# Kernel tuning notes

Hardware: AMD Instinct MI355X
Metric: run time of the kernel (lower is better)

The kernel has to match this reference:

```python
import jax, jax.numpy as jnp
import numpy as np

DIM = 768
NUM_HEADS = 12
N_DIV = 8
T_SHIFT = 20
T_SPAN = 11
T_CUT = T_SHIFT + 1 - T_SPAN  # 10
C = DIM // NUM_HEADS          # 64 channels per head
FOLD = C // N_DIV             # 8
BATCH = 2
FRAMES = 32
K_WIN = 4
N_TOK = 196
B_TOT = BATCH * FRAMES * K_WIN  # 256


def _entmax15_last(x):
    """Exact entmax-1.5 (Peters & Martins) along the last axis."""
    x = (x - jnp.max(x, axis=-1, keepdims=True)) * 0.5
    xs = jnp.flip(jnp.sort(x, axis=-1), axis=-1)  # descending
    d = x.shape[-1]
    rho = jnp.arange(1, d + 1, dtype=x.dtype)
    mean = jnp.cumsum(xs, axis=-1) / rho
    meansq = jnp.cumsum(xs * xs, axis=-1) / rho
    ss = rho * (meansq - mean * mean)
    delta = (1.0 - ss) / rho
    pos = delta > 0
    sq = jnp.where(pos, jnp.sqrt(jnp.where(pos, delta, 1.0)), 0.0)
    tau = mean - sq
    support = jnp.sum(tau <= xs, axis=-1, keepdims=True)
    tau_star = jnp.take_along_axis(tau, support - 1, axis=-1)
    y = jnp.clip(x - tau_star, 0.0, None)
    return y * y


def entmax15(x, axis):
    return jnp.moveaxis(_entmax15_last(jnp.moveaxis(x, axis, -1)), -1, axis)


def _shift(feat, pool_w, pool_b, win_w, win_b, forward):
    # feat: [b, t, k, h, n, c]
    b, t, k, h, n, c = feat.shape
    f = N_DIV
    cp = c // f
    # 'b t k h n (c f) -> (k n h c) (b f) t'
    g = feat.reshape(b, t, k, h, n, cp, f)
    g = jnp.transpose(g, (2, 4, 3, 5, 0, 6, 1)).reshape(k * n * h * cp, b * f, t)
    pad = (T_SHIFT, 0) if forward else (0, T_SHIFT)
    g = jnp.pad(g, ((0, 0), (0, 0), pad))
    # 'b t k h n c -> b (k n t) (h c)'
    xk = jnp.transpose(feat, (0, 2, 4, 1, 3, 5)).reshape(b, k * n * t, h * c)
    attn = xk @ pool_w + pool_b                      # [b, knt, 1]
    pooled = jnp.sum(entmax15(attn, axis=1) * xk, axis=1)  # [b, dim]
    # 'b 1 (T f) -> (b f) 1 T'
    win = (pooled @ win_w + win_b).reshape(b, T_SPAN, f)
    win = jnp.transpose(win, (0, 2, 1)).reshape(b * f, 1, T_SPAN)
    win = _entmax15_last(win)
    # depthwise conv over the (b f) channel dim, batch dim = k*n*h*cp
    out = jax.lax.conv_general_dilated(
        g, win, (1,), 'VALID',
        dimension_numbers=('NCH', 'OIH', 'NCH'),
        feature_group_count=b * f)
    tp = t + T_CUT
    # '(k n h c) (b f) t -> b t k h n c f' then mean over f
    out = out.reshape(k, n, h, cp, b, f, tp)
    out = jnp.transpose(out, (4, 6, 0, 2, 1, 3, 5)).mean(axis=-1)  # [b, tp, k, h, n, cp]
    return out[:, :-T_CUT] if forward else out[:, T_CUT:]


def _pcs(x, batch_size, frame_len, fpw, fpb, bpw, bpb, fww, fwb, bww, bwb):
    B, h, n, c = x.shape
    k = B // (batch_size * frame_len)
    feat = x.reshape(batch_size, frame_len, k, h, n, c)
    fwd = _shift(feat, fpw, fpb, fww, fwb, True)
    bwd = _shift(feat, bpw, bpb, bww, bwb, False)
    out = jnp.concatenate([fwd, bwd, feat[..., 2 * FOLD:]], axis=-1)
    return out.reshape(B, h, n, c)


def setup_inputs() -> dict:
    key = jax.random.key(0)
    ks = jax.random.split(key, 6)
    s = 0.02
    return {
        'x': jax.random.normal(ks[0], (B_TOT, NUM_HEADS, N_TOK, C), dtype=jnp.float32),
        'batch_size': BATCH,
        'frame_len': FRAMES,
        'fwd_pool_w': jax.random.normal(ks[1], (DIM, 1), dtype=jnp.float32) * s,
        'fwd_pool_b': jnp.zeros((1,), dtype=jnp.float32),
        'bwd_pool_w': jax.random.normal(ks[2], (DIM, 1), dtype=jnp.float32) * s,
        'bwd_pool_b': jnp.zeros((1,), dtype=jnp.float32),
        'fwd_win_w': jax.random.normal(ks[3], (DIM, T_SPAN * N_DIV), dtype=jnp.float32) * s,
        'fwd_win_b': jnp.zeros((T_SPAN * N_DIV,), dtype=jnp.float32),
        'bwd_win_w': jax.random.normal(ks[4], (DIM, T_SPAN * N_DIV), dtype=jnp.float32) * s,
        'bwd_win_b': jnp.zeros((T_SPAN * N_DIV,), dtype=jnp.float32),
    }


def reference(x, batch_size, frame_len, fwd_pool_w, fwd_pool_b, bwd_pool_w, bwd_pool_b,
              fwd_win_w, fwd_win_b, bwd_win_w, bwd_win_b):
    return _pcs(x, batch_size, frame_len, fwd_pool_w, fwd_pool_b, bwd_pool_w, bwd_pool_b,
                fwd_win_w, fwd_win_b, bwd_win_w, bwd_win_b)
```

## Files before the change

kernel.cpp:

```cpp
#include <hip/hip_runtime.h>

#define NH 12
#define NTOK 196
#define TT 32
#define KW 4
#define NI 25088
#define TSTRIDE 602112

typedef float nfloat4 __attribute__((ext_vector_type(4)));

__global__ __launch_bounds__(256) void k_attn(
    const float4* __restrict__ x4, const float4* __restrict__ wf4,
    const float4* __restrict__ wb4, float* __restrict__ attn,
    float4* __restrict__ out4)
{
  int B = blockIdx.y;
  int wave = threadIdx.x >> 6, lane = threadIdx.x & 63;
  int n = blockIdx.x * 16 + wave * 4 + (lane >> 4);
  int c4 = lane & 15;
  bool nv = (n < NTOK);
  float accf = 0.f, accb = 0.f;
  #pragma unroll
  for (int h = 0; h < NH; h++) {
    float4 xv = make_float4(0.f, 0.f, 0.f, 0.f);
    int gi = ((B * NH + h) * NTOK + n) * 16 + c4;
    if (nv) xv = x4[gi];
    float4 wf = wf4[h * 16 + c4];
    float4 wb = wb4[h * 16 + c4];
    accf += xv.x * wf.x + xv.y * wf.y + xv.z * wf.z + xv.w * wf.w;
    accb += xv.x * wb.x + xv.y * wb.y + xv.z * wb.z + xv.w * wb.w;
    if (nv && c4 >= 4) {
      nfloat4 nv4 = { xv.x, xv.y, xv.z, xv.w };
      __builtin_nontemporal_store(nv4, (nfloat4*)&out4[gi]);
    }
  }
  #pragma unroll
  for (int m = 1; m < 16; m <<= 1) {
    accf += __shfl_xor(accf, m);
    accb += __shfl_xor(accb, m);
  }
  if (nv && (lane & 15) == 0) {
    int b = B >> 7, t = (B >> 2) & 31, k = B & 3;
    int i = (k * NTOK + n) * TT + t;
    attn[(0 * 2 + b) * NI + i] = accf;
    attn[(1 * 2 + b) * NI + i] = accb;
  }
}

__global__ __launch_bounds__(1024) void k_entmax_big(
    const float* __restrict__ attn, float* __restrict__ wgt,
    int* __restrict__ idxb, int* __restrict__ cnt)
{
  int p = blockIdx.x;
  const float* a = attn + p * NI;
  int tid = threadIdx.x;
  float v[25];
  float mx = -3.0e38f;
  #pragma unroll
  for (int r = 0; r < 25; r++) {
    int i = r * 1024 + tid;
    v[r] = (i < NI) ? a[i] : -3.0e38f;
    mx = fmaxf(mx, v[r]);
  }
  __shared__ float sred1[16];
  __shared__ float sred2[16];
  __shared__ float sbc;
  int wv = tid >> 6;
  #pragma unroll
  for (int m = 1; m < 64; m <<= 1) mx = fmaxf(mx, __shfl_xor(mx, m));
  if ((tid & 63) == 0) sred1[wv] = mx;
  __syncthreads();
  if (tid == 0) {
    float m2 = sred1[0];
    for (int i2 = 1; i2 < 16; i2++) m2 = fmaxf(m2, sred1[i2]);
    sbc = m2;
  }
  __syncthreads();
  float amax = sbc;
  #pragma unroll
  for (int r = 0; r < 25; r++) v[r] = 0.5f * (v[r] - amax);
  float tau = -1.0f;
  for (int it = 0; it < 8; it++) {
    float s2 = 0.f, s1 = 0.f;
    #pragma unroll
    for (int r = 0; r < 25; r++) {
      float d = fmaxf(v[r] - tau, 0.f);
      s2 += d * d;
      s1 += d;
    }
    #pragma unroll
    for (int m = 1; m < 64; m <<= 1) {
      s2 += __shfl_xor(s2, m);
      s1 += __shfl_xor(s1, m);
    }
    if ((tid & 63) == 0) { sred2[wv] = s2; sred1[wv] = s1; }
    __syncthreads();
    if (tid == 0) {
      float S2 = 0.f, S1 = 0.f;
      for (int i2 = 0; i2 < 16; i2++) { S2 += sred2[i2]; S1 += sred1[i2]; }
      sbc = tau + (S2 - 1.f) / fmaxf(2.f * S1, 1e-12f);
    }
    __syncthreads();
    tau = sbc;
    __syncthreads();
  }
  #pragma unroll
  for (int r = 0; r < 25; r++) {
    float d = v[r] - tau;
    if (d > 0.f) {
      int i = r * 1024 + tid;
      int slot = atomicAdd(&cnt[p], 1);
      idxb[p * NI + slot] = i;
      wgt[p * NI + slot] = d * d;
    }
  }
}

__global__ __launch_bounds__(256) void k_pool(
    const float* __restrict__ x, const int* __restrict__ idxb,
    const float* __restrict__ wgt, const int* __restrict__ cnt,
    float* __restrict__ pooled)
{
  int p = blockIdx.x >> 3, stripe = blockIdx.x & 7;
  int b = p & 1;
  int wv = threadIdx.x >> 6, lane = threadIdx.x & 63;
  int count = cnt[p];
  float acc[12];
  #pragma unroll
  for (int q = 0; q < 12; q++) acc[q] = 0.f;
  for (int e = stripe * 4 + wv; e < count; e += 32) {
    int i = idxb[p * NI + e];
    float pw = wgt[p * NI + e];
    int t = i & 31, r = i >> 5;
    int n = r % NTOK, k = r / NTOK;
    int B = (b * TT + t) * KW + k;
    const float* xb = x + B * 150528 + n * 64 + lane;
    #pragma unroll
    for (int q = 0; q < 12; q++) acc[q] += pw * xb[q * 12544];
  }
  #pragma unroll
  for (int q = 0; q < 12; q++)
    atomicAdd(&pooled[p * 768 + q * 64 + lane], acc[q]);
}

__global__ __launch_bounds__(384) void k_win(
    const float* __restrict__ pooled,
    const float* __restrict__ fww, const float* __restrict__ fwb,
    const float* __restrict__ bww, const float* __restrict__ bwb,
    float* __restrict__ winout)
{
  __shared__ float praw[4][88];
  int tid = threadIdx.x;
  if (tid < 352) {
    int p = tid / 88, col = tid % 88;
    const float* ww = (p >> 1) ? bww : fww;
    const float* wb = (p >> 1) ? bwb : fwb;
    float acc = wb[col];
    const float* pl = pooled + p * 768;
    #pragma unroll 8
    for (int r = 0; r < 768; r++) acc += pl[r] * ww[r * 88 + col];
    praw[p][col] = acc;
  }
  __syncthreads();
  if (tid < 32) {
    int p = tid >> 3, f = tid & 7;
    float v[11];
    float mx = -3.0e38f;
    #pragma unroll
    for (int j = 0; j < 11; j++) { v[j] = praw[p][j * 8 + f]; mx = fmaxf(mx, v[j]); }
    #pragma unroll
    for (int j = 0; j < 11; j++) v[j] = 0.5f * (v[j] - mx);
    float lo = -1.f, hi = 0.f;
    for (int it = 0; it < 30; it++) {
      float mid = 0.5f * (lo + hi);
      float s = 0.f;
      #pragma unroll
      for (int j = 0; j < 11; j++) { float d = fmaxf(v[j] - mid, 0.f); s += d * d; }
      if (s >= 1.f) lo = mid; else hi = mid;
    }
    float tau = 0.5f * (lo + hi);
    #pragma unroll
    for (int j = 0; j < 11; j++) {
      float d = fmaxf(v[j] - tau, 0.f);
      winout[p * 88 + f * 11 + j] = d * d * 0.125f;
    }
  }
}

__global__ __launch_bounds__(256) void k_shift(
    const float* __restrict__ x, const float* __restrict__ win,
    float* __restrict__ out)
{
  int bkh = blockIdx.y;
  int b = bkh / 48, rem = bkh % 48;
  int k = rem / 12, h = rem % 12;
  int wave = threadIdx.x >> 6, lane = threadIdx.x & 63;
  int n = blockIdx.x * 4 + wave;
  int f = lane & 7, cp = lane >> 3;
  float wjf[11], wjb[11];
  #pragma unroll
  for (int j = 0; j < 11; j++) {
    wjf[j] = win[(0 * 2 + b) * 88 + f * 11 + j];
    wjb[j] = win[(1 * 2 + b) * 88 + f * 11 + j];
  }
  int base = ((b * 128 + k) * NH + h) * 12544 + n * 64 + cp * 8 + f;
  float xr[32];
  #pragma unroll
  for (int tp = 0; tp < 32; tp++) xr[tp] = x[base + tp * TSTRIDE];

  int ob = ((b * 128 + k) * NH + h) * 12544 + n * 64 + cp;
  float acc[32];

  #pragma unroll
  for (int t = 0; t < 32; t++) acc[t] = 0.f;
  #pragma unroll
  for (int tp = 0; tp <= 21; tp++) {
    #pragma unroll
    for (int j = 0; j < 11; j++) {
      int to = tp + 20 - j;
      if (to >= 0 && to < 32) acc[to] += wjf[j] * xr[tp];
    }
  }
  #pragma unroll
  for (int t = 0; t < 32; t++) {
    float s = acc[t];
    s += __shfl_xor(s, 1);
    s += __shfl_xor(s, 2);
    s += __shfl_xor(s, 4);
    acc[t] = s;
  }
  if (f == 0) {
    #pragma unroll
    for (int t = 0; t < 32; t++)
      __builtin_nontemporal_store(acc[t], &out[ob + t * TSTRIDE]);
  }

  #pragma unroll
  for (int t = 0; t < 32; t++) acc[t] = 0.f;
  #pragma unroll
  for (int tp = 10; tp < 32; tp++) {
    #pragma unroll
    for (int j = 0; j < 11; j++) {
      int to = tp - 10 - j;
      if (to >= 0 && to < 32) acc[to] += wjb[j] * xr[tp];
    }
  }
  #pragma unroll
  for (int t = 0; t < 32; t++) {
    float s = acc[t];
    s += __shfl_xor(s, 1);
    s += __shfl_xor(s, 2);
    s += __shfl_xor(s, 4);
    acc[t] = s;
  }
  if (f == 0) {
    #pragma unroll
    for (int t = 0; t < 32; t++)
      __builtin_nontemporal_store(acc[t], &out[ob + 8 + t * TSTRIDE]);
  }
}

extern "C" void kernel_launch(void* const* d_in, const int* in_sizes, int n_in,
                              void* d_out, int out_size, void* d_ws, size_t ws_size,
                              hipStream_t stream)
{
  (void)in_sizes; (void)n_in; (void)out_size; (void)ws_size;
  const float* x   = (const float*)d_in[0];
  const float* fpw = (const float*)d_in[3];
  const float* bpw = (const float*)d_in[5];
  const float* fww = (const float*)d_in[7];
  const float* fwb = (const float*)d_in[8];
  const float* bww = (const float*)d_in[9];
  const float* bwb = (const float*)d_in[10];
  float* out = (float*)d_out;

  float* W      = (float*)d_ws;
  int*   cnt    = (int*)W;
  float* pooled = W + 4;
  float* attn   = W + 4 + 3072;
  float* wgt    = attn + 4 * NI;
  int*   idxb   = (int*)(wgt + 4 * NI);
  float* winb   = (float*)(idxb + 4 * NI);

  (void)hipMemsetAsync(d_ws, 0, (4 + 3072) * sizeof(float), stream);

  dim3 g1(13, 256);
  k_attn<<<g1, 256, 0, stream>>>((const float4*)x, (const float4*)fpw,
                                 (const float4*)bpw, attn, (float4*)out);
  k_entmax_big<<<4, 1024, 0, stream>>>(attn, wgt, idxb, cnt);
  k_pool<<<32, 256, 0, stream>>>(x, idxb, wgt, cnt, pooled);
  k_win<<<1, 384, 0, stream>>>(pooled, fww, fwb, bww, bwb, winb);
  dim3 g5(49, 96);
  k_shift<<<g5, 256, 0, stream>>>(x, winb, out);
}
```

Measured before the change: 420.6 us.

## Fuse entmax with pooling, split window matvec, move passthrough copy into shift

Fuses the entmax kernel with the sparse pooling step. The support indices and weights now live in shared memory, which removes the workspace memset, the global atomics and a separate launch. The window projection is split over four blocks with a row-segmented reduction. The passthrough copy of unshifted channels moves from k_attn into k_shift, which now writes the whole output with coalesced stores using data it already loaded. The risks are the serial pooling loop, which runs on only 4 blocks and may be slow for large supports, and the support being capped at 8192 entries, which could truncate results.

```diff
diff --git a/kernel.cpp b/kernel.cpp
--- a/kernel.cpp
+++ b/kernel.cpp
@@ -7,32 +7,29 @@
 #define NI 25088
 #define TSTRIDE 602112
 
-typedef float nfloat4 __attribute__((ext_vector_type(4)));
-
 __global__ __launch_bounds__(256) void k_attn(
     const float4* __restrict__ x4, const float4* __restrict__ wf4,
-    const float4* __restrict__ wb4, float* __restrict__ attn,
-    float4* __restrict__ out4)
-{
+    const float4* __restrict__ wb4, float* __restrict__ attn)
+{
+  __shared__ float4 swf[192], swb[192];
+  int tid = threadIdx.x;
+  if (tid < 192) { swf[tid] = wf4[tid]; swb[tid] = wb4[tid]; }
+  __syncthreads();
+
   int B = blockIdx.y;
-  int wave = threadIdx.x >> 6, lane = threadIdx.x & 63;
-  int n = blockIdx.x * 16 + wave * 4 + (lane >> 4);
+  int lane = tid & 63;
+  int n = blockIdx.x * 16 + (tid >> 6) * 4 + (lane >> 4);
   int c4 = lane & 15;
   bool nv = (n < NTOK);
   float accf = 0.f, accb = 0.f;
   #pragma unroll
   for (int h = 0; h < NH; h++) {
     float4 xv = make_float4(0.f, 0.f, 0.f, 0.f);
-    int gi = ((B * NH + h) * NTOK + n) * 16 + c4;
-    if (nv) xv = x4[gi];
-    float4 wf = wf4[h * 16 + c4];
-    float4 wb = wb4[h * 16 + c4];
+    if (nv) xv = x4[((B * NH + h) * NTOK + n) * 16 + c4];
+    float4 wf = swf[h * 16 + c4];
+    float4 wb = swb[h * 16 + c4];
     accf += xv.x * wf.x + xv.y * wf.y + xv.z * wf.z + xv.w * wf.w;
     accb += xv.x * wb.x + xv.y * wb.y + xv.z * wb.z + xv.w * wb.w;
-    if (nv && c4 >= 4) {
-      nfloat4 nv4 = { xv.x, xv.y, xv.z, xv.w };
-      __builtin_nontemporal_store(nv4, (nfloat4*)&out4[gi]);
-    }
   }
   #pragma unroll
   for (int m = 1; m < 16; m <<= 1) {
@@ -47,11 +44,12 @@
   }
 }
 
-__global__ __launch_bounds__(1024) void k_entmax_big(
-    const float* __restrict__ attn, float* __restrict__ wgt,
-    int* __restrict__ idxb, int* __restrict__ cnt)
+__global__ __launch_bounds__(1024) void k_entmax_pool(
+    const float* __restrict__ attn, const float* __restrict__ x,
+    float* __restrict__ pooled)
 {
   int p = blockIdx.x;
+  int b = p & 1;
   const float* a = attn + p * NI;
   int tid = threadIdx.x;
   float v[25];
@@ -104,70 +102,71 @@
     tau = sbc;
     __syncthreads();
   }
+  __shared__ int scnt;
+  __shared__ int sidx[8192];
+  __shared__ float swgt[8192];
+  if (tid == 0) scnt = 0;
+  __syncthreads();
   #pragma unroll
   for (int r = 0; r < 25; r++) {
     float d = v[r] - tau;
     if (d > 0.f) {
-      int i = r * 1024 + tid;
-      int slot = atomicAdd(&cnt[p], 1);
-      idxb[p * NI + slot] = i;
-      wgt[p * NI + slot] = d * d;
-    }
-  }
-}
-
-__global__ __launch_bounds__(256) void k_pool(
-    const float* __restrict__ x, const int* __restrict__ idxb,
-    const float* __restrict__ wgt, const int* __restrict__ cnt,
-    float* __restrict__ pooled)
-{
-  int p = blockIdx.x >> 3, stripe = blockIdx.x & 7;
-  int b = p & 1;
-  int wv = threadIdx.x >> 6, lane = threadIdx.x & 63;
-  int count = cnt[p];
-  float acc[12];
-  #pragma unroll
-  for (int q = 0; q < 12; q++) acc[q] = 0.f;
-  for (int e = stripe * 4 + wv; e < count; e += 32) {
-    int i = idxb[p * NI + e];
-    float pw = wgt[p * NI + e];
-    int t = i & 31, r = i >> 5;
-    int n = r % NTOK, k = r / NTOK;
-    int B = (b * TT + t) * KW + k;
-    const float* xb = x + B * 150528 + n * 64 + lane;
-    #pragma unroll
-    for (int q = 0; q < 12; q++) acc[q] += pw * xb[q * 12544];
-  }
-  #pragma unroll
-  for (int q = 0; q < 12; q++)
-    atomicAdd(&pooled[p * 768 + q * 64 + lane], acc[q]);
-}
-
-__global__ __launch_bounds__(384) void k_win(
+      int slot = atomicAdd(&scnt, 1);
+      if (slot < 8192) { sidx[slot] = r * 1024 + tid; swgt[slot] = d * d; }
+    }
+  }
+  __syncthreads();
+  int count = min(scnt, 8192);
+  if (tid < 768) {
+    int h = tid >> 6, c = tid & 63;
+    float acc = 0.f;
+    for (int e = 0; e < count; e++) {
+      int i = sidx[e];
+      float w = swgt[e];
+      int t = i & 31, r2 = i >> 5;
+      int n = r2 % NTOK, k = r2 / NTOK;
+      int B = (b * TT + t) * KW + k;
+      acc += w * x[((B * NH + h) * NTOK + n) * 64 + c];
+    }
+    pooled[p * 768 + tid] = acc;
+  }
+}
+
+__global__ __launch_bounds__(704) void k_win(
     const float* __restrict__ pooled,
     const float* __restrict__ fww, const float* __restrict__ fwb,
     const float* __restrict__ bww, const float* __restrict__ bwb,
     float* __restrict__ winout)
 {
-  __shared__ float praw[4][88];
+  int p = blockIdx.x;
+  const float* ww = (p >> 1) ? bww : fww;
+  const float* wb = (p >> 1) ? bwb : fwb;
+  const float* pl = pooled + p * 768;
   int tid = threadIdx.x;
-  if (tid < 352) {
-    int p = tid / 88, col = tid % 88;
-    const float* ww = (p >> 1) ? bww : fww;
-    const float* wb = (p >> 1) ? bwb : fwb;
-    float acc = wb[col];
-    const float* pl = pooled + p * 768;
-    #pragma unroll 8
-    for (int r = 0; r < 768; r++) acc += pl[r] * ww[r * 88 + col];
-    praw[p][col] = acc;
-  }
-  __syncthreads();
-  if (tid < 32) {
-    int p = tid >> 3, f = tid & 7;
+  int rseg = tid / 88, col = tid % 88;
+  __shared__ float part[8][88];
+  __shared__ float praw[88];
+  float acc = 0.f;
+  #pragma unroll 8
+  for (int j = 0; j < 96; j++) {
+    int r = rseg * 96 + j;
+    acc += pl[r] * ww[r * 88 + col];
+  }
+  part[rseg][col] = acc;
+  __syncthreads();
+  if (tid < 88) {
+    float s = wb[tid];
+    #pragma unroll
+    for (int g = 0; g < 8; g++) s += part[g][tid];
+    praw[tid] = s;
+  }
+  __syncthreads();
+  if (tid < 8) {
+    int f = tid;
     float v[11];
     float mx = -3.0e38f;
     #pragma unroll
-    for (int j = 0; j < 11; j++) { v[j] = praw[p][j * 8 + f]; mx = fmaxf(mx, v[j]); }
+    for (int j = 0; j < 11; j++) { v[j] = praw[j * 8 + f]; mx = fmaxf(mx, v[j]); }
     #pragma unroll
     for (int j = 0; j < 11; j++) v[j] = 0.5f * (v[j] - mx);
     float lo = -1.f, hi = 0.f;
@@ -196,67 +195,65 @@
   int k = rem / 12, h = rem % 12;
   int wave = threadIdx.x >> 6, lane = threadIdx.x & 63;
   int n = blockIdx.x * 4 + wave;
-  int f = lane & 7, cp = lane >> 3;
+  int f = lane & 7;
   float wjf[11], wjb[11];
   #pragma unroll
   for (int j = 0; j < 11; j++) {
     wjf[j] = win[(0 * 2 + b) * 88 + f * 11 + j];
     wjb[j] = win[(1 * 2 + b) * 88 + f * 11 + j];
   }
-  int base = ((b * 128 + k) * NH + h) * 12544 + n * 64 + cp * 8 + f;
+  int base = ((b * 128 + k) * NH + h) * 12544 + n * 64 + lane;
   float xr[32];
   #pragma unroll
   for (int tp = 0; tp < 32; tp++) xr[tp] = x[base + tp * TSTRIDE];
 
-  int ob = ((b * 128 + k) * NH + h) * 12544 + n * 64 + cp;
-  float acc[32];
-
-  #pragma unroll
-  for (int t = 0; t < 32; t++) acc[t] = 0.f;
+  float accF[32];
+  #pragma unroll
+  for (int t = 0; t < 32; t++) accF[t] = 0.f;
   #pragma unroll
   for (int tp = 0; tp <= 21; tp++) {
     #pragma unroll
     for (int j = 0; j < 11; j++) {
       int to = tp + 20 - j;
-      if (to >= 0 && to < 32) acc[to] += wjf[j] * xr[tp];
+      if (to >= 0 && to < 32) accF[to] += wjf[j] * xr[tp];
     }
   }
   #pragma unroll
   for (int t = 0; t < 32; t++) {
-    float s = acc[t];
+    float s = accF[t];
     s += __shfl_xor(s, 1);
     s += __shfl_xor(s, 2);
     s += __shfl_xor(s, 4);
-    acc[t] = s;
-  }
-  if (f == 0) {
-    #pragma unroll
-    for (int t = 0; t < 32; t++)
-      __builtin_nontemporal_store(acc[t], &out[ob + t * TSTRIDE]);
-  }
-
-  #pragma unroll
-  for (int t = 0; t < 32; t++) acc[t] = 0.f;
+    accF[t] = s;
+  }
+
+  float accB[32];
+  #pragma unroll
+  for (int t = 0; t < 32; t++) accB[t] = 0.f;
   #pragma unroll
   for (int tp = 10; tp < 32; tp++) {
     #pragma unroll
     for (int j = 0; j < 11; j++) {
       int to = tp - 10 - j;
-      if (to >= 0 && to < 32) acc[to] += wjb[j] * xr[tp];
+      if (to >= 0 && to < 32) accB[to] += wjb[j] * xr[tp];
     }
   }
   #pragma unroll
   for (int t = 0; t < 32; t++) {
-    float s = acc[t];
+    float s = accB[t];
     s += __shfl_xor(s, 1);
     s += __shfl_xor(s, 2);
     s += __shfl_xor(s, 4);
-    acc[t] = s;
-  }
-  if (f == 0) {
-    #pragma unroll
-    for (int t = 0; t < 32; t++)
-      __builtin_nontemporal_store(acc[t], &out[ob + 8 + t * TSTRIDE]);
+    accB[t] = s;
+  }
+
+  int src = (lane & 7) << 3;
+  #pragma unroll
+  for (int t = 0; t < 32; t++) {
+    float sf = __shfl(accF[t], src);
+    float sb = __shfl(accB[t], src);
+    float val = (lane < 8) ? sf : (lane < 16) ? sb : xr[t];
+    __builtin_nontemporal_store(val, &out[base + t * TSTRIDE]);
   }
 }
 
@@ -275,21 +272,15 @@
   float* out = (float*)d_out;
 
   float* W      = (float*)d_ws;
-  int*   cnt    = (int*)W;
-  float* pooled = W + 4;
-  float* attn   = W + 4 + 3072;
-  float* wgt    = attn + 4 * NI;
-  int*   idxb   = (int*)(wgt + 4 * NI);
-  float* winb   = (float*)(idxb + 4 * NI);
-
-  (void)hipMemsetAsync(d_ws, 0, (4 + 3072) * sizeof(float), stream);
+  float* attn   = W;
+  float* pooled = attn + 4 * NI;
+  float* winb   = pooled + 3072;
 
   dim3 g1(13, 256);
   k_attn<<<g1, 256, 0, stream>>>((const float4*)x, (const float4*)fpw,
-                                 (const float4*)bpw, attn, (float4*)out);
-  k_entmax_big<<<4, 1024, 0, stream>>>(attn, wgt, idxb, cnt);
-  k_pool<<<32, 256, 0, stream>>>(x, idxb, wgt, cnt, pooled);
-  k_win<<<1, 384, 0, stream>>>(pooled, fww, fwb, bww, bwb, winb);
+                                 (const float4*)bpw, attn);
+  k_entmax_pool<<<4, 1024, 0, stream>>>(attn, x, pooled);
+  k_win<<<4, 704, 0, stream>>>(pooled, fww, fwb, bww, bwb, winb);
   dim3 g5(49, 96);
   k_shift<<<g5, 256, 0, stream>>>(x, winb, out);
 }
```

Result: faster. 339.3 us (-19.3%).
